# Kernel optimization log

Hardware: AMD Instinct MI355X
Metric: run time of the kernel (lower is better)

Reference implementation:

```python
import jax, jax.numpy as jnp
import numpy as np

N = 16384      # nodes
E = 524288     # edges (avg degree 32)
F_IN = 128     # input features
H1 = 256       # first_gcn_dimensions
H2 = 256       # second_gcn_dimensions
D1 = 64        # first_dense_neurons
D2 = 2         # second_dense_neurons (fixed by EYE=ones(2))


def setup_inputs() -> dict:
    key = jax.random.key(0)
    ks = jax.random.split(key, 8)
    w = lambda k, shp: (jax.random.normal(k, shp, jnp.float32) * 0.05)
    return dict(
        features=jax.random.normal(ks[0], (N, F_IN), jnp.float32),
        edges=jax.random.randint(ks[1], (2, E), 0, N),
        W1=w(ks[2], (F_IN, H1)), b1=jnp.zeros((H1,), jnp.float32),
        W2=w(ks[3], (H1, H2)), b2=jnp.zeros((H2,), jnp.float32),
        fc1_w=w(ks[4], (D1, H2)), fc1_b=jnp.zeros((D1,), jnp.float32),
        fc2_w=w(ks[5], (D2, D1)), fc2_b=jnp.zeros((D2,), jnp.float32),
    )


def gcn_conv(x, W, b, src, dst, n):
    """PyG GCNConv: xW, add self-loops, symmetric D^-1/2 (A+I) D^-1/2 aggregation."""
    x = x @ W
    loops = jnp.arange(n)
    s = jnp.concatenate([src, loops])
    d = jnp.concatenate([dst, loops])
    deg = jax.ops.segment_sum(jnp.ones(s.shape, x.dtype), d, num_segments=n)
    dinv = jnp.where(deg > 0, jax.lax.rsqrt(deg), 0.0)
    msg = x[s] * (dinv[s] * dinv[d])[:, None]          # gather + scale
    return jax.ops.segment_sum(msg, d, num_segments=n) + b  # scatter-add


def reference(features, edges, W1, b1, W2, b2, fc1_w, fc1_b, fc2_w, fc2_b):
    n = features.shape[0]
    src, dst = edges[0], edges[1]
    h1 = jax.nn.relu(gcn_conv(features, W1, b1, src, dst, n))
    h2 = gcn_conv(h1, W2, b2, src, dst, n)                 # [N, H2]
    a1 = jnp.tanh(h2 @ fc1_w.T + fc1_b)                    # [N, D1]
    assignment = jax.nn.softmax(a1 @ fc2_w.T + fc2_b, axis=1)  # [N, 2]
    group_features = assignment.T @ h2                     # [2, H2]
    # to_dense_adj: dense NxN adjacency, duplicate edges accumulate
    adj = jnp.zeros((n, n), h2.dtype).at[src, dst].add(1.0)
    new_adj = assignment.T @ (adj @ assignment)            # [2, 2]
    positive = jnp.clip(group_features[0][None, :], -100.0, 100.0)
    negative = jnp.clip(group_features[1][None, :], -100.0, 100.0)
    # F.normalize(p=1, dim=1) with eps=1e-12
    denom = jnp.maximum(jnp.sum(jnp.abs(new_adj), axis=1, keepdims=True), 1e-12)
    norm_diag = jnp.diag(new_adj / denom)
    pos_penalty = jnp.mean((norm_diag - 1.0) ** 2)         # MSE vs ones(2)
    graph_embedding = jnp.mean(group_features, axis=0, keepdims=True)  # [1, H2]
    return (graph_embedding, positive, negative, pos_penalty)
```

## Files before the change

kernel.cpp:

```cpp
#include <hip/hip_runtime.h>
#include <hip/hip_bf16.h>
#include <hip/hip_fp8.h>
#include <math.h>

#define N_NODES 16384
#define N_EDGES 524288
#define F_IN 128
#define H1 256
#define H2 256
#define D1 64
#define NA_GRID 512
#define DEG_CAP 96
#define SENT 16384

typedef __attribute__((ext_vector_type(8))) short short8;
typedef __attribute__((ext_vector_type(4))) float floatx4;
typedef unsigned short ushort_t;
typedef unsigned int uint_t;
typedef unsigned char uchar_t;

__device__ inline float bf2f(ushort_t u) {
    union { uint_t i; float f; } v;
    v.i = ((uint_t)u) << 16;
    return v.f;
}
__device__ inline ushort_t f2bs(float x) {
    __hip_bfloat16 h = __float2bfloat16(x);
    return *reinterpret_cast<ushort_t*>(&h);
}
__device__ inline uint_t pack2(float lo, float hi) {
    return (uint_t)f2bs(lo) | ((uint_t)f2bs(hi) << 16);
}
__device__ inline float f8tof(uint_t b) {
    __hip_fp8_e4m3 h; h.__x = (__hip_fp8_storage_t)(b & 0xff);
    return (float)h;
}
__device__ inline uint_t ftof8(float v) {
    __hip_fp8_e4m3 h(v);
    return (uint_t)h.__x;
}

__global__ __launch_bounds__(256) void prep_fill(
    const int* __restrict__ src, const int* __restrict__ dst,
    const float* __restrict__ W1, const float* __restrict__ W2,
    const float* __restrict__ fc1_w,
    int* __restrict__ cur, ushort_t* __restrict__ col,
    ushort_t* __restrict__ W1t, ushort_t* __restrict__ W2t,
    ushort_t* __restrict__ fc1bf) {
    int b = blockIdx.x, t = threadIdx.x;
    if (b < 2048) {
        int e = b * 256 + t;
        int d = dst[e];
        int pos = atomicAdd(&cur[d], 1);
        if (pos < DEG_CAP) col[d * DEG_CAP + pos] = (ushort_t)src[e];
    } else if (b < 2176) {
        int idx = (b - 2048) * 256 + t;
        int n = idx >> 7, k = idx & 127;
        W1t[idx] = f2bs(W1[k * 256 + n]);
    } else if (b < 2432) {
        int idx = (b - 2176) * 256 + t;
        int n = idx >> 8, k = idx & 255;
        W2t[idx] = f2bs(W2[k * 256 + n]);
    } else {
        int idx = (b - 2432) * 256 + t;
        fc1bf[idx] = f2bs(fc1_w[idx]);
    }
}

__global__ __launch_bounds__(256) void scale_feat(
    const float* __restrict__ features, const int* __restrict__ cnt,
    uchar_t* __restrict__ zs8, uchar_t* __restrict__ bufY8,
    ushort_t* __restrict__ col) {
    int b = blockIdx.x, t = threadIdx.x;
    if (b == 2048) {
        uint4 z4 = {0u, 0u, 0u, 0u};
        if (t < 8)
            *(uint4*)&zs8[(size_t)SENT * 128 + t * 16] = z4;
        else if (t >= 64 && t < 80)
            *(uint4*)&bufY8[(size_t)SENT * 256 + (t - 64) * 16] = z4;
        return;
    }
    int gid = b * 256 + t;
    int node = gid >> 5;
    int hl = gid & 31;
    int deg = cnt[node];
    float d = rsqrtf((float)(deg + 1));
    float4 v = *(const float4*)&features[gid * 4];
    uint_t p = ftof8(v.x * d) | (ftof8(v.y * d) << 8) |
               (ftof8(v.z * d) << 16) | (ftof8(v.w * d) << 24);
    *(uint_t*)&zs8[gid * 4] = p;
    if (deg < DEG_CAP) {
        int pad = (16 - (deg & 15)) & 15;
        if (hl < pad) col[node * DEG_CAP + deg + hl] = (ushort_t)SENT;
    }
}

__global__ __launch_bounds__(512, 4) void fused_layer1(
    const uchar_t* __restrict__ zs8, const int* __restrict__ cnt,
    const ushort_t* __restrict__ col, const float* __restrict__ b1,
    const ushort_t* __restrict__ W1t, const ushort_t* __restrict__ W2t,
    uchar_t* __restrict__ bufY8) {
    __shared__ __align__(16) ushort_t Az[16 * 136];
    __shared__ __align__(16) ushort_t Ah[16 * 264];
    __shared__ __align__(8) uint_t scol[768];
    const int tid = threadIdx.x;
    const int lane = tid & 63;
    const int wave = tid >> 6;
    const int m = lane & 15;
    const int quad = lane >> 4;
    const int row0 = blockIdx.x * 16;
    const uint_t* colu = (const uint_t*)col;

    if (tid < 384)
        *(uint2*)&scol[tid * 2] = *(const uint2*)&colu[row0 * 48 + tid * 2];
    __syncthreads();

    {
        const int nl0 = wave * 2, nl1 = wave * 2 + 1;
        const int node0 = row0 + nl0, node1 = row0 + nl1;
        const int foff = lane * 2;
        const int deg0 = cnt[node0], deg1 = cnt[node1];
        const int nb0 = (min(deg0, DEG_CAP) + 15) >> 4;
        const int nb1 = (min(deg1, DEG_CAP) + 15) >> 4;
        const int nbm = max(nb0, nb1);
        ushort_t s0 = *(const ushort_t*)&zs8[(size_t)node0 * 128 + foff];
        ushort_t s1 = *(const ushort_t*)&zs8[(size_t)node1 * 128 + foff];
        float a00 = f8tof(s0), a01 = f8tof(s0 >> 8);
        float a10 = f8tof(s1), a11 = f8tof(s1 >> 8);
        for (int tb = 0; tb < nbm; ++tb) {
            const bool p0 = tb < nb0, p1 = tb < nb1;
            uint_t w0[8], w1[8];
            if (p0) {
                #pragma unroll
                for (int k = 0; k < 8; ++k) w0[k] = scol[nl0 * 48 + tb * 8 + k];
            }
            if (p1) {
                #pragma unroll
                for (int k = 0; k < 8; ++k) w1[k] = scol[nl1 * 48 + tb * 8 + k];
            }
            ushort_t g0[16], g1[16];
            if (p0) {
                #pragma unroll
                for (int k = 0; k < 8; ++k) {
                    int j0 = w0[k] & 0xffff, j1 = w0[k] >> 16;
                    g0[2 * k]     = *(const ushort_t*)&zs8[(size_t)j0 * 128 + foff];
                    g0[2 * k + 1] = *(const ushort_t*)&zs8[(size_t)j1 * 128 + foff];
                }
            }
            if (p1) {
                #pragma unroll
                for (int k = 0; k < 8; ++k) {
                    int j0 = w1[k] & 0xffff, j1 = w1[k] >> 16;
                    g1[2 * k]     = *(const ushort_t*)&zs8[(size_t)j0 * 128 + foff];
                    g1[2 * k + 1] = *(const ushort_t*)&zs8[(size_t)j1 * 128 + foff];
                }
            }
            if (p0) {
                #pragma unroll
                for (int q = 0; q < 16; ++q) {
                    a00 += f8tof(g0[q]); a01 += f8tof(g0[q] >> 8);
                }
            }
            if (p1) {
                #pragma unroll
                for (int q = 0; q < 16; ++q) {
                    a10 += f8tof(g1[q]); a11 += f8tof(g1[q] >> 8);
                }
            }
        }
        float dn0 = rsqrtf((float)(deg0 + 1));
        float dn1 = rsqrtf((float)(deg1 + 1));
        *(uint_t*)&Az[nl0 * 136 + foff] = pack2(a00 * dn0, a01 * dn0);
        *(uint_t*)&Az[nl1 * 136 + foff] = pack2(a10 * dn1, a11 * dn1);
    }
    __syncthreads();

    const int wcol0 = wave * 32;
    floatx4 acc[2];
    const floatx4 zero4 = {0.f, 0.f, 0.f, 0.f};
    acc[0] = zero4; acc[1] = zero4;
    #pragma unroll
    for (int k0 = 0; k0 < 128; k0 += 32) {
        short8 a = *(const short8*)&Az[m * 136 + k0 + quad * 8];
        #pragma unroll
        for (int j = 0; j < 2; ++j) {
            short8 bb = *(const short8*)
                &W1t[(size_t)(wcol0 + j * 16 + m) * 128 + k0 + quad * 8];
            acc[j] = __builtin_amdgcn_mfma_f32_16x16x32_bf16(a, bb, acc[j], 0, 0, 0);
        }
    }
    #pragma unroll
    for (int j = 0; j < 2; ++j) {
        int cg = wcol0 + j * 16 + m;
        float bv = b1[cg];
        #pragma unroll
        for (int r = 0; r < 4; ++r) {
            float v = fmaxf(acc[j][r] + bv, 0.0f);
            Ah[(quad * 4 + r) * 264 + cg] = f2bs(v);
        }
    }
    __syncthreads();

    acc[0] = zero4; acc[1] = zero4;
    #pragma unroll
    for (int k0 = 0; k0 < 256; k0 += 32) {
        short8 a = *(const short8*)&Ah[m * 264 + k0 + quad * 8];
        #pragma unroll
        for (int j = 0; j < 2; ++j) {
            short8 bb = *(const short8*)
                &W2t[(size_t)(wcol0 + j * 16 + m) * 256 + k0 + quad * 8];
            acc[j] = __builtin_amdgcn_mfma_f32_16x16x32_bf16(a, bb, acc[j], 0, 0, 0);
        }
    }
    float rs4[4];
    #pragma unroll
    for (int r = 0; r < 4; ++r)
        rs4[r] = rsqrtf((float)(cnt[row0 + quad * 4 + r] + 1));
    #pragma unroll
    for (int j = 0; j < 2; ++j) {
        int cg = wcol0 + j * 16 + m;
        #pragma unroll
        for (int r = 0; r < 4; ++r)
            bufY8[(size_t)(row0 + quad * 4 + r) * 256 + cg] =
                (uchar_t)ftof8(acc[j][r] * rs4[r]);
    }
}

__global__ __launch_bounds__(512, 4) void fused_assign(
    const uchar_t* __restrict__ bufY8, const int* __restrict__ cnt,
    const ushort_t* __restrict__ col, const float* __restrict__ b2,
    const ushort_t* __restrict__ fc1bf, const float* __restrict__ fc1_b,
    const float* __restrict__ fc2_w, const float* __restrict__ fc2_b,
    float* __restrict__ assignp, float* __restrict__ gfr) {
    __shared__ __align__(16) ushort_t Ah[16 * 264];
    __shared__ __align__(8) uint_t scol[768];
    __shared__ float sha[16][65];
    __shared__ float sas0[16], sas1[16];
    const int tid = threadIdx.x;
    const int lane = tid & 63;
    const int wave = tid >> 6;
    const int m = lane & 15;
    const int quad = lane >> 4;
    const int row0 = blockIdx.x * 16;
    const uint_t* colu = (const uint_t*)col;

    if (tid < 384)
        *(uint2*)&scol[tid * 2] = *(const uint2*)&colu[row0 * 48 + tid * 2];
    __syncthreads();

    {
        const int nl0 = wave * 2, nl1 = wave * 2 + 1;
        const int node0 = row0 + nl0, node1 = row0 + nl1;
        const int foff = lane * 4;
        const int deg0 = cnt[node0], deg1 = cnt[node1];
        const int nb0 = (min(deg0, DEG_CAP) + 15) >> 4;
        const int nb1 = (min(deg1, DEG_CAP) + 15) >> 4;
        const int nbm = max(nb0, nb1);
        uint_t sv0 = *(const uint_t*)&bufY8[(size_t)node0 * 256 + foff];
        uint_t sv1 = *(const uint_t*)&bufY8[(size_t)node1 * 256 + foff];
        float a00 = f8tof(sv0),       a01 = f8tof(sv0 >> 8);
        float a02 = f8tof(sv0 >> 16), a03 = f8tof(sv0 >> 24);
        float a10 = f8tof(sv1),       a11 = f8tof(sv1 >> 8);
        float a12 = f8tof(sv1 >> 16), a13 = f8tof(sv1 >> 24);
        for (int tb = 0; tb < nbm; ++tb) {
            const bool p0 = tb < nb0, p1 = tb < nb1;
            uint_t w0[8], w1[8];
            if (p0) {
                #pragma unroll
                for (int k = 0; k < 8; ++k) w0[k] = scol[nl0 * 48 + tb * 8 + k];
            }
            if (p1) {
                #pragma unroll
                for (int k = 0; k < 8; ++k) w1[k] = scol[nl1 * 48 + tb * 8 + k];
            }
            uint_t g0[16], g1[16];
            if (p0) {
                #pragma unroll
                for (int k = 0; k < 8; ++k) {
                    int j0 = w0[k] & 0xffff, j1 = w0[k] >> 16;
                    g0[2 * k]     = *(const uint_t*)&bufY8[(size_t)j0 * 256 + foff];
                    g0[2 * k + 1] = *(const uint_t*)&bufY8[(size_t)j1 * 256 + foff];
                }
            }
            if (p1) {
                #pragma unroll
                for (int k = 0; k < 8; ++k) {
                    int j0 = w1[k] & 0xffff, j1 = w1[k] >> 16;
                    g1[2 * k]     = *(const uint_t*)&bufY8[(size_t)j0 * 256 + foff];
                    g1[2 * k + 1] = *(const uint_t*)&bufY8[(size_t)j1 * 256 + foff];
                }
            }
            if (p0) {
                #pragma unroll
                for (int q = 0; q < 16; ++q) {
                    a00 += f8tof(g0[q]);       a01 += f8tof(g0[q] >> 8);
                    a02 += f8tof(g0[q] >> 16); a03 += f8tof(g0[q] >> 24);
                }
            }
            if (p1) {
                #pragma unroll
                for (int q = 0; q < 16; ++q) {
                    a10 += f8tof(g1[q]);       a11 += f8tof(g1[q] >> 8);
                    a12 += f8tof(g1[q] >> 16); a13 += f8tof(g1[q] >> 24);
                }
            }
        }
        float di0 = rsqrtf((float)(deg0 + 1));
        float di1 = rsqrtf((float)(deg1 + 1));
        float4 bv = *(const float4*)&b2[foff];
        uint2 pk;
        pk.x = pack2(a00 * di0 + bv.x, a01 * di0 + bv.y);
        pk.y = pack2(a02 * di0 + bv.z, a03 * di0 + bv.w);
        *(uint2*)&Ah[nl0 * 264 + foff] = pk;
        pk.x = pack2(a10 * di1 + bv.x, a11 * di1 + bv.y);
        pk.y = pack2(a12 * di1 + bv.z, a13 * di1 + bv.w);
        *(uint2*)&Ah[nl1 * 264 + foff] = pk;
    }
    __syncthreads();

    if (wave < 4) {
        floatx4 acc = {0.f, 0.f, 0.f, 0.f};
        #pragma unroll
        for (int k0 = 0; k0 < 256; k0 += 32) {
            short8 a = *(const short8*)&Ah[m * 264 + k0 + quad * 8];
            short8 bb = *(const short8*)
                &fc1bf[(size_t)(wave * 16 + m) * 256 + k0 + quad * 8];
            acc = __builtin_amdgcn_mfma_f32_16x16x32_bf16(a, bb, acc, 0, 0, 0);
        }
        int cg = wave * 16 + m;
        float bv = fc1_b[cg];
        #pragma unroll
        for (int r = 0; r < 4; ++r)
            sha[quad * 4 + r][cg] = tanhf(acc[r] + bv);
    }
    __syncthreads();

    if (tid < 16) {
        float p0 = fc2_b[0], p1 = fc2_b[1];
        #pragma unroll 8
        for (int t = 0; t < 64; ++t) {
            float a = sha[tid][t];
            p0 += a * fc2_w[t];
            p1 += a * fc2_w[64 + t];
        }
        float mx = fmaxf(p0, p1);
        float e0 = expf(p0 - mx), e1 = expf(p1 - mx);
        float inv = 1.0f / (e0 + e1);
        assignp[row0 + tid] = e0 * inv;
        sas0[tid] = e0 * inv; sas1[tid] = e1 * inv;
    }
    __syncthreads();

    {
        const int f = tid & 255;
        const int which = tid >> 8;
        const float* sv = which ? sas1 : sas0;
        float acc = 0.f;
        #pragma unroll
        for (int i = 0; i < 16; ++i)
            acc += sv[i] * bf2f(Ah[i * 264 + f]);
        float* gfc = gfr + (blockIdx.x & 3) * 512;
        atomicAdd(&gfc[which * 256 + f], acc);
    }
}

__global__ __launch_bounds__(256) void newadj_fin(
    const int* __restrict__ src, const int* __restrict__ dst,
    const float* __restrict__ assignp, float* __restrict__ napart,
    int* __restrict__ cntt, const float* __restrict__ gfr,
    float* __restrict__ out) {
    __shared__ float red[4][3];
    __shared__ int sticket;
    const int tid = threadIdx.x;
    const int b = blockIdx.x;
    const int lane = tid & 63;
    const int wave = tid >> 6;

    float ss = 0.f, sd = 0.f, ssd = 0.f;
    {
        int g = (b * 256 + tid) * 4;
        int4 sv = *(const int4*)&src[g];
        int4 dv = *(const int4*)&dst[g];
        float s0 = assignp[sv.x], s1 = assignp[sv.y];
        float s2 = assignp[sv.z], s3 = assignp[sv.w];
        float d0 = assignp[dv.x], d1 = assignp[dv.y];
        float d2 = assignp[dv.z], d3 = assignp[dv.w];
        ss = s0 + s1 + s2 + s3;
        sd = d0 + d1 + d2 + d3;
        ssd = s0 * d0 + s1 * d1 + s2 * d2 + s3 * d3;
    }
    #pragma unroll
    for (int off = 32; off; off >>= 1) {
        ss += __shfl_down(ss, off);
        sd += __shfl_down(sd, off);
        ssd += __shfl_down(ssd, off);
    }
    if (lane == 0) {
        red[wave][0] = ssd; red[wave][1] = ss; red[wave][2] = sd;
    }
    __syncthreads();
    if (tid < 3) {
        float v = red[0][tid] + red[1][tid] + red[2][tid] + red[3][tid];
        __hip_atomic_store(&napart[b * 4 + tid], v, __ATOMIC_RELEASE,
                           __HIP_MEMORY_SCOPE_AGENT);
    }
    __syncthreads();
    if (tid == 0)
        sticket = __hip_atomic_fetch_add(cntt, 1, __ATOMIC_ACQ_REL,
                                         __HIP_MEMORY_SCOPE_AGENT);
    __syncthreads();
    if (sticket != NA_GRID - 1) return;

    float acc = 0.f;
    if (wave < 3) {
        for (int i = lane; i < NA_GRID; i += 64)
            acc += __hip_atomic_load(&napart[i * 4 + wave], __ATOMIC_RELAXED,
                                     __HIP_MEMORY_SCOPE_AGENT);
    }
    #pragma unroll
    for (int off = 32; off; off >>= 1) acc += __shfl_down(acc, off);
    __shared__ float na[3];
    if (lane == 0 && wave < 3) na[wave] = acc;
    __syncthreads();
    float g0 = gfr[tid] + gfr[512 + tid] + gfr[1024 + tid] + gfr[1536 + tid];
    float g1 = gfr[256 + tid] + gfr[768 + tid] + gfr[1280 + tid] + gfr[1792 + tid];
    out[tid] = 0.5f * (g0 + g1);
    out[256 + tid] = fminf(fmaxf(g0, -100.f), 100.f);
    out[512 + tid] = fminf(fmaxf(g1, -100.f), 100.f);
    if (tid == 0) {
        float Ssd = na[0], Ss = na[1], Sd = na[2];
        float n00 = Ssd;
        float n01 = Ss - Ssd;
        float n10 = Sd - Ssd;
        float n11 = (float)N_EDGES - Ss - Sd + Ssd;
        float den0 = fmaxf(fabsf(n00) + fabsf(n01), 1e-12f);
        float den1 = fmaxf(fabsf(n10) + fabsf(n11), 1e-12f);
        float x0 = n00 / den0 - 1.0f;
        float x1 = n11 / den1 - 1.0f;
        out[768] = 0.5f * (x0 * x0 + x1 * x1);
    }
}


extern "C" void kernel_launch(void* const* d_in, const int* in_sizes, int n_in,
                              void* d_out, int out_size, void* d_ws, size_t ws_size,
                              hipStream_t stream) {
    const float* features = (const float*)d_in[0];
    const int* edges = (const int*)d_in[1];
    const int* src = edges;
    const int* dst = edges + N_EDGES;
    const float* W1 = (const float*)d_in[2];
    const float* b1 = (const float*)d_in[3];
    const float* W2 = (const float*)d_in[4];
    const float* b2 = (const float*)d_in[5];
    const float* fc1_w = (const float*)d_in[6];
    const float* fc1_b = (const float*)d_in[7];
    const float* fc2_w = (const float*)d_in[8];
    const float* fc2_b = (const float*)d_in[9];
    float* out = (float*)d_out;

    char* ws = (char*)d_ws;
    auto carve = [&](size_t bytes) {
        void* q = (void*)ws;
        ws += (bytes + 255) & ~(size_t)255;
        return q;
    };
    int* cur = (int*)carve(N_NODES * 4);
    float* gfr = (float*)carve(4 * 512 * 4);
    int* cnt_na = (int*)carve(256);
    ushort_t* col = (ushort_t*)carve((size_t)N_NODES * DEG_CAP * 2);
    float* assignp = (float*)carve(N_NODES * 4);
    float* napart = (float*)carve(NA_GRID * 4 * 4);
    ushort_t* fc1bf = (ushort_t*)carve(64 * 256 * 2);
    uchar_t* zs8 = (uchar_t*)carve((size_t)(N_NODES + 1) * F_IN);
    ushort_t* W1t = (ushort_t*)carve(256 * 128 * 2);
    ushort_t* W2t = (ushort_t*)carve(256 * 256 * 2);
    uchar_t* bufY8 = (uchar_t*)carve((size_t)(N_NODES + 1) * 256);

    hipMemsetAsync(cur, 0, N_NODES * 4 + 4 * 512 * 4 + 256, stream);

    prep_fill<<<2496, 256, 0, stream>>>(src, dst, W1, W2, fc1_w,
                                        cur, col, W1t, W2t, fc1bf);
    scale_feat<<<2049, 256, 0, stream>>>(features, cur, zs8, bufY8, col);
    fused_layer1<<<N_NODES / 16, 512, 0, stream>>>(
        zs8, cur, col, b1, W1t, W2t, bufY8);
    fused_assign<<<N_NODES / 16, 512, 0, stream>>>(
        bufY8, cur, col, b2, fc1bf, fc1_b, fc2_w, fc2_b, assignp, gfr);
    newadj_fin<<<NA_GRID, 256, 0, stream>>>(src, dst, assignp, napart,
                                            cnt_na, gfr, out);
}
```

Before: 187.9 us.

## Fuse all stages into one cooperative persistent kernel with grid syncs

Replaces the memset plus five separate kernel launches with a single cooperative kernel of 256 blocks. The stages are CSR fill, weight conversion, feature scaling, layer1+layer2 GEMM, assignment, and the new-adjacency reduction and finalize, separated by grid.sync(). This removes launch gaps and the memset. In exchange, each persistent block loops over tiles, which reduces parallelism per stage, and six grid-wide barriers are added. The old multi-kernel path is kept as a fallback if the cooperative launch fails.

```diff
diff --git a/kernel.cpp b/kernel.cpp
--- a/kernel.cpp
+++ b/kernel.cpp
@@ -1,7 +1,10 @@
 #include <hip/hip_runtime.h>
+#include <hip/hip_cooperative_groups.h>
 #include <hip/hip_bf16.h>
 #include <hip/hip_fp8.h>
 #include <math.h>
+
+namespace cg = cooperative_groups;
 
 #define N_NODES 16384
 #define N_EDGES 524288
@@ -12,6 +15,9 @@
 #define NA_GRID 512
 #define DEG_CAP 96
 #define SENT 16384
+#define NBLK 256
+#define NTHR 512
+#define NTH (NBLK * NTHR)
 
 typedef __attribute__((ext_vector_type(8))) short short8;
 typedef __attribute__((ext_vector_type(4))) float floatx4;
@@ -39,6 +45,393 @@
     __hip_fp8_e4m3 h(v);
     return (uint_t)h.__x;
 }
+
+__global__ __launch_bounds__(512, 4) void mega(
+    const int* __restrict__ src, const int* __restrict__ dst,
+    const float* __restrict__ features,
+    const float* __restrict__ W1, const float* __restrict__ b1,
+    const float* __restrict__ W2, const float* __restrict__ b2,
+    const float* __restrict__ fc1_w, const float* __restrict__ fc1_b,
+    const float* __restrict__ fc2_w, const float* __restrict__ fc2_b,
+    int* __restrict__ cur, ushort_t* __restrict__ col,
+    float* __restrict__ assignp, float* __restrict__ napart,
+    ushort_t* __restrict__ fc1bf, uchar_t* __restrict__ zs8,
+    ushort_t* __restrict__ W1t, ushort_t* __restrict__ W2t,
+    uchar_t* __restrict__ bufY8, float* __restrict__ gfr,
+    float* __restrict__ out) {
+    cg::grid_group grid = cg::this_grid();
+    __shared__ __align__(16) ushort_t Az[16 * 136];
+    __shared__ __align__(16) ushort_t Ah[16 * 264];
+    __shared__ __align__(8) uint_t scol[768];
+    __shared__ float sha[16][65];
+    __shared__ float sas0[16], sas1[16];
+    __shared__ float red[8][3];
+
+    const int tid = threadIdx.x;
+    const int gid = blockIdx.x * NTHR + tid;
+    const int lane = tid & 63;
+    const int wave = tid >> 6;
+    const int m = lane & 15;
+    const int quad = lane >> 4;
+    const uint_t* colu = (const uint_t*)col;
+
+    if (gid < N_NODES) cur[gid] = 0;
+    else if (gid < N_NODES + 2048) gfr[gid - N_NODES] = 0.f;
+    grid.sync();
+
+    for (int e = gid; e < N_EDGES; e += NTH) {
+        int d = dst[e];
+        int pos = atomicAdd(&cur[d], 1);
+        if (pos < DEG_CAP) col[d * DEG_CAP + pos] = (ushort_t)src[e];
+    }
+    if (gid < 114688) {
+        int i = gid;
+        if (i < 32768) {
+            int n = i >> 7, k = i & 127;
+            W1t[i] = f2bs(W1[k * 256 + n]);
+        } else if (i < 98304) {
+            int j = i - 32768;
+            int n = j >> 8, k = j & 255;
+            W2t[j] = f2bs(W2[k * 256 + n]);
+        } else {
+            int j = i - 98304;
+            fc1bf[j] = f2bs(fc1_w[j]);
+        }
+    }
+    grid.sync();
+
+    if (gid < 8) {
+        uint4 z4 = {0u, 0u, 0u, 0u};
+        *(uint4*)&zs8[(size_t)SENT * 128 + gid * 16] = z4;
+    } else if (gid >= 64 && gid < 80) {
+        uint4 z4 = {0u, 0u, 0u, 0u};
+        *(uint4*)&bufY8[(size_t)SENT * 256 + (gid - 64) * 16] = z4;
+    }
+    for (int i = gid; i < 524288; i += NTH) {
+        int node = i >> 5;
+        int hl = i & 31;
+        int deg = cur[node];
+        float d = rsqrtf((float)(deg + 1));
+        float4 v = *(const float4*)&features[i * 4];
+        uint_t p = ftof8(v.x * d) | (ftof8(v.y * d) << 8) |
+                   (ftof8(v.z * d) << 16) | (ftof8(v.w * d) << 24);
+        *(uint_t*)&zs8[i * 4] = p;
+        if (deg < DEG_CAP) {
+            int pad = (16 - (deg & 15)) & 15;
+            if (hl < pad) col[node * DEG_CAP + deg + hl] = (ushort_t)SENT;
+        }
+    }
+    grid.sync();
+
+    for (int tl = blockIdx.x; tl < N_NODES / 16; tl += NBLK) {
+        const int row0 = tl * 16;
+        if (tid < 384)
+            *(uint2*)&scol[tid * 2] = *(const uint2*)&colu[row0 * 48 + tid * 2];
+        __syncthreads();
+        {
+            const int nl0 = wave * 2, nl1 = wave * 2 + 1;
+            const int node0 = row0 + nl0, node1 = row0 + nl1;
+            const int foff = lane * 2;
+            const int deg0 = cur[node0], deg1 = cur[node1];
+            const int nb0 = (min(deg0, DEG_CAP) + 15) >> 4;
+            const int nb1 = (min(deg1, DEG_CAP) + 15) >> 4;
+            const int nbm = max(nb0, nb1);
+            ushort_t s0 = *(const ushort_t*)&zs8[(size_t)node0 * 128 + foff];
+            ushort_t s1 = *(const ushort_t*)&zs8[(size_t)node1 * 128 + foff];
+            float a00 = f8tof(s0), a01 = f8tof(s0 >> 8);
+            float a10 = f8tof(s1), a11 = f8tof(s1 >> 8);
+            for (int tb = 0; tb < nbm; ++tb) {
+                const bool p0 = tb < nb0, p1 = tb < nb1;
+                uint_t w0[8], w1[8];
+                if (p0) {
+                    #pragma unroll
+                    for (int k = 0; k < 8; ++k) w0[k] = scol[nl0 * 48 + tb * 8 + k];
+                }
+                if (p1) {
+                    #pragma unroll
+                    for (int k = 0; k < 8; ++k) w1[k] = scol[nl1 * 48 + tb * 8 + k];
+                }
+                ushort_t g0[16], g1[16];
+                if (p0) {
+                    #pragma unroll
+                    for (int k = 0; k < 8; ++k) {
+                        int j0 = w0[k] & 0xffff, j1 = w0[k] >> 16;
+                        g0[2 * k]     = *(const ushort_t*)&zs8[(size_t)j0 * 128 + foff];
+                        g0[2 * k + 1] = *(const ushort_t*)&zs8[(size_t)j1 * 128 + foff];
+                    }
+                }
+                if (p1) {
+                    #pragma unroll
+                    for (int k = 0; k < 8; ++k) {
+                        int j0 = w1[k] & 0xffff, j1 = w1[k] >> 16;
+                        g1[2 * k]     = *(const ushort_t*)&zs8[(size_t)j0 * 128 + foff];
+                        g1[2 * k + 1] = *(const ushort_t*)&zs8[(size_t)j1 * 128 + foff];
+                    }
+                }
+                if (p0) {
+                    #pragma unroll
+                    for (int q = 0; q < 16; ++q) {
+                        a00 += f8tof(g0[q]); a01 += f8tof(g0[q] >> 8);
+                    }
+                }
+                if (p1) {
+                    #pragma unroll
+                    for (int q = 0; q < 16; ++q) {
+                        a10 += f8tof(g1[q]); a11 += f8tof(g1[q] >> 8);
+                    }
+                }
+            }
+            float dn0 = rsqrtf((float)(deg0 + 1));
+            float dn1 = rsqrtf((float)(deg1 + 1));
+            *(uint_t*)&Az[nl0 * 136 + foff] = pack2(a00 * dn0, a01 * dn0);
+            *(uint_t*)&Az[nl1 * 136 + foff] = pack2(a10 * dn1, a11 * dn1);
+        }
+        __syncthreads();
+        const int wcol0 = wave * 32;
+        floatx4 acc[2];
+        const floatx4 zero4 = {0.f, 0.f, 0.f, 0.f};
+        acc[0] = zero4; acc[1] = zero4;
+        #pragma unroll
+        for (int k0 = 0; k0 < 128; k0 += 32) {
+            short8 a = *(const short8*)&Az[m * 136 + k0 + quad * 8];
+            #pragma unroll
+            for (int j = 0; j < 2; ++j) {
+                short8 bb = *(const short8*)
+                    &W1t[(size_t)(wcol0 + j * 16 + m) * 128 + k0 + quad * 8];
+                acc[j] = __builtin_amdgcn_mfma_f32_16x16x32_bf16(a, bb, acc[j], 0, 0, 0);
+            }
+        }
+        #pragma unroll
+        for (int j = 0; j < 2; ++j) {
+            int cg_ = wcol0 + j * 16 + m;
+            float bv = b1[cg_];
+            #pragma unroll
+            for (int r = 0; r < 4; ++r) {
+                float v = fmaxf(acc[j][r] + bv, 0.0f);
+                Ah[(quad * 4 + r) * 264 + cg_] = f2bs(v);
+            }
+        }
+        __syncthreads();
+        acc[0] = zero4; acc[1] = zero4;
+        #pragma unroll
+        for (int k0 = 0; k0 < 256; k0 += 32) {
+            short8 a = *(const short8*)&Ah[m * 264 + k0 + quad * 8];
+            #pragma unroll
+            for (int j = 0; j < 2; ++j) {
+                short8 bb = *(const short8*)
+                    &W2t[(size_t)(wcol0 + j * 16 + m) * 256 + k0 + quad * 8];
+                acc[j] = __builtin_amdgcn_mfma_f32_16x16x32_bf16(a, bb, acc[j], 0, 0, 0);
+            }
+        }
+        float rs4[4];
+        #pragma unroll
+        for (int r = 0; r < 4; ++r)
+            rs4[r] = rsqrtf((float)(cur[row0 + quad * 4 + r] + 1));
+        #pragma unroll
+        for (int j = 0; j < 2; ++j) {
+            int cg_ = wcol0 + j * 16 + m;
+            #pragma unroll
+            for (int r = 0; r < 4; ++r)
+                bufY8[(size_t)(row0 + quad * 4 + r) * 256 + cg_] =
+                    (uchar_t)ftof8(acc[j][r] * rs4[r]);
+        }
+        __syncthreads();
+    }
+    grid.sync();
+
+    for (int tl = blockIdx.x; tl < N_NODES / 16; tl += NBLK) {
+        const int row0 = tl * 16;
+        if (tid < 384)
+            *(uint2*)&scol[tid * 2] = *(const uint2*)&colu[row0 * 48 + tid * 2];
+        __syncthreads();
+        {
+            const int nl0 = wave * 2, nl1 = wave * 2 + 1;
+            const int node0 = row0 + nl0, node1 = row0 + nl1;
+            const int foff = lane * 4;
+            const int deg0 = cur[node0], deg1 = cur[node1];
+            const int nb0 = (min(deg0, DEG_CAP) + 15) >> 4;
+            const int nb1 = (min(deg1, DEG_CAP) + 15) >> 4;
+            const int nbm = max(nb0, nb1);
+            uint_t sv0 = *(const uint_t*)&bufY8[(size_t)node0 * 256 + foff];
+            uint_t sv1 = *(const uint_t*)&bufY8[(size_t)node1 * 256 + foff];
+            float a00 = f8tof(sv0),       a01 = f8tof(sv0 >> 8);
+            float a02 = f8tof(sv0 >> 16), a03 = f8tof(sv0 >> 24);
+            float a10 = f8tof(sv1),       a11 = f8tof(sv1 >> 8);
+            float a12 = f8tof(sv1 >> 16), a13 = f8tof(sv1 >> 24);
+            for (int tb = 0; tb < nbm; ++tb) {
+                const bool p0 = tb < nb0, p1 = tb < nb1;
+                uint_t w0[8], w1[8];
+                if (p0) {
+                    #pragma unroll
+                    for (int k = 0; k < 8; ++k) w0[k] = scol[nl0 * 48 + tb * 8 + k];
+                }
+                if (p1) {
+                    #pragma unroll
+                    for (int k = 0; k < 8; ++k) w1[k] = scol[nl1 * 48 + tb * 8 + k];
+                }
+                uint_t g0[16], g1[16];
+                if (p0) {
+                    #pragma unroll
+                    for (int k = 0; k < 8; ++k) {
+                        int j0 = w0[k] & 0xffff, j1 = w0[k] >> 16;
+                        g0[2 * k]     = *(const uint_t*)&bufY8[(size_t)j0 * 256 + foff];
+                        g0[2 * k + 1] = *(const uint_t*)&bufY8[(size_t)j1 * 256 + foff];
+                    }
+                }
+                if (p1) {
+                    #pragma unroll
+                    for (int k = 0; k < 8; ++k) {
+                        int j0 = w1[k] & 0xffff, j1 = w1[k] >> 16;
+                        g1[2 * k]     = *(const uint_t*)&bufY8[(size_t)j0 * 256 + foff];
+                        g1[2 * k + 1] = *(const uint_t*)&bufY8[(size_t)j1 * 256 + foff];
+                    }
+                }
+                if (p0) {
+                    #pragma unroll
+                    for (int q = 0; q < 16; ++q) {
+                        a00 += f8tof(g0[q]);       a01 += f8tof(g0[q] >> 8);
+                        a02 += f8tof(g0[q] >> 16); a03 += f8tof(g0[q] >> 24);
+                    }
+                }
+                if (p1) {
+                    #pragma unroll
+                    for (int q = 0; q < 16; ++q) {
+                        a10 += f8tof(g1[q]);       a11 += f8tof(g1[q] >> 8);
+                        a12 += f8tof(g1[q] >> 16); a13 += f8tof(g1[q] >> 24);
+                    }
+                }
+            }
+            float di0 = rsqrtf((float)(deg0 + 1));
+            float di1 = rsqrtf((float)(deg1 + 1));
+            float4 bv = *(const float4*)&b2[foff];
+            uint2 pk;
+            pk.x = pack2(a00 * di0 + bv.x, a01 * di0 + bv.y);
+            pk.y = pack2(a02 * di0 + bv.z, a03 * di0 + bv.w);
+            *(uint2*)&Ah[nl0 * 264 + foff] = pk;
+            pk.x = pack2(a10 * di1 + bv.x, a11 * di1 + bv.y);
+            pk.y = pack2(a12 * di1 + bv.z, a13 * di1 + bv.w);
+            *(uint2*)&Ah[nl1 * 264 + foff] = pk;
+        }
+        __syncthreads();
+        if (wave < 4) {
+            floatx4 acc = {0.f, 0.f, 0.f, 0.f};
+            #pragma unroll
+            for (int k0 = 0; k0 < 256; k0 += 32) {
+                short8 a = *(const short8*)&Ah[m * 264 + k0 + quad * 8];
+                short8 bb = *(const short8*)
+                    &fc1bf[(size_t)(wave * 16 + m) * 256 + k0 + quad * 8];
+                acc = __builtin_amdgcn_mfma_f32_16x16x32_bf16(a, bb, acc, 0, 0, 0);
+            }
+            int cg_ = wave * 16 + m;
+            float bv = fc1_b[cg_];
+            #pragma unroll
+            for (int r = 0; r < 4; ++r)
+                sha[quad * 4 + r][cg_] = tanhf(acc[r] + bv);
+        }
+        __syncthreads();
+        if (tid < 16) {
+            float p0 = fc2_b[0], p1 = fc2_b[1];
+            #pragma unroll 8
+            for (int t = 0; t < 64; ++t) {
+                float a = sha[tid][t];
+                p0 += a * fc2_w[t];
+                p1 += a * fc2_w[64 + t];
+            }
+            float mx = fmaxf(p0, p1);
+            float e0 = expf(p0 - mx), e1 = expf(p1 - mx);
+            float inv = 1.0f / (e0 + e1);
+            assignp[row0 + tid] = e0 * inv;
+            sas0[tid] = e0 * inv; sas1[tid] = e1 * inv;
+        }
+        __syncthreads();
+        {
+            const int f = tid & 255;
+            const int which = tid >> 8;
+            const float* sv = which ? sas1 : sas0;
+            float acc = 0.f;
+            #pragma unroll
+            for (int i = 0; i < 16; ++i)
+                acc += sv[i] * bf2f(Ah[i * 264 + f]);
+            float* gfc = gfr + ((tl >> 2) & 3) * 512;
+            atomicAdd(&gfc[which * 256 + f], acc);
+        }
+        __syncthreads();
+    }
+    grid.sync();
+
+    {
+        int g4 = gid * 4;
+        int4 sv = *(const int4*)&src[g4];
+        int4 dv = *(const int4*)&dst[g4];
+        float s0 = assignp[sv.x], s1 = assignp[sv.y];
+        float s2 = assignp[sv.z], s3 = assignp[sv.w];
+        float d0 = assignp[dv.x], d1 = assignp[dv.y];
+        float d2 = assignp[dv.z], d3 = assignp[dv.w];
+        float ss = s0 + s1 + s2 + s3;
+        float sd = d0 + d1 + d2 + d3;
+        float ssd = s0 * d0 + s1 * d1 + s2 * d2 + s3 * d3;
+        #pragma unroll
+        for (int off = 32; off; off >>= 1) {
+            ss += __shfl_down(ss, off);
+            sd += __shfl_down(sd, off);
+            ssd += __shfl_down(ssd, off);
+        }
+        if (lane == 0) {
+            red[wave][0] = ssd; red[wave][1] = ss; red[wave][2] = sd;
+        }
+        __syncthreads();
+        if (tid < 3) {
+            float v = 0.f;
+            #pragma unroll
+            for (int w = 0; w < 8; ++w) v += red[w][tid];
+            napart[blockIdx.x * 4 + tid] = v;
+        }
+    }
+    grid.sync();
+
+    if (blockIdx.x == 0) {
+        float p0 = 0.f, p1 = 0.f, p2 = 0.f;
+        if (tid < NBLK) {
+            p0 = napart[tid * 4];
+            p1 = napart[tid * 4 + 1];
+            p2 = napart[tid * 4 + 2];
+        }
+        #pragma unroll
+        for (int off = 32; off; off >>= 1) {
+            p0 += __shfl_down(p0, off);
+            p1 += __shfl_down(p1, off);
+            p2 += __shfl_down(p2, off);
+        }
+        if (lane == 0) {
+            red[wave][0] = p0; red[wave][1] = p1; red[wave][2] = p2;
+        }
+        __syncthreads();
+        if (tid < 256) {
+            float g0 = gfr[tid] + gfr[512 + tid] + gfr[1024 + tid] + gfr[1536 + tid];
+            float g1 = gfr[256 + tid] + gfr[768 + tid] + gfr[1280 + tid] + gfr[1792 + tid];
+            out[tid] = 0.5f * (g0 + g1);
+            out[256 + tid] = fminf(fmaxf(g0, -100.f), 100.f);
+            out[512 + tid] = fminf(fmaxf(g1, -100.f), 100.f);
+        }
+        if (tid == 0) {
+            float Ssd = 0.f, Ss = 0.f, Sd = 0.f;
+            #pragma unroll
+            for (int w = 0; w < 8; ++w) {
+                Ssd += red[w][0]; Ss += red[w][1]; Sd += red[w][2];
+            }
+            float n00 = Ssd;
+            float n01 = Ss - Ssd;
+            float n10 = Sd - Ssd;
+            float n11 = (float)N_EDGES - Ss - Sd + Ssd;
+            float den0 = fmaxf(fabsf(n00) + fabsf(n01), 1e-12f);
+            float den1 = fmaxf(fabsf(n10) + fabsf(n11), 1e-12f);
+            float x0 = n00 / den0 - 1.0f;
+            float x1 = n11 / den1 - 1.0f;
+            out[768] = 0.5f * (x0 * x0 + x1 * x1);
+        }
+    }
+}
+
 
 __global__ __launch_bounds__(256) void prep_fill(
     const int* __restrict__ src, const int* __restrict__ dst,
@@ -114,7 +507,6 @@
     if (tid < 384)
         *(uint2*)&scol[tid * 2] = *(const uint2*)&colu[row0 * 48 + tid * 2];
     __syncthreads();
-
     {
         const int nl0 = wave * 2, nl1 = wave * 2 + 1;
         const int node0 = row0 + nl0, node1 = row0 + nl1;
@@ -174,7 +566,6 @@
         *(uint_t*)&Az[nl1 * 136 + foff] = pack2(a10 * dn1, a11 * dn1);
     }
     __syncthreads();
-
     const int wcol0 = wave * 32;
     floatx4 acc[2];
     const floatx4 zero4 = {0.f, 0.f, 0.f, 0.f};
@@ -191,16 +582,15 @@
     }
     #pragma unroll
     for (int j = 0; j < 2; ++j) {
-        int cg = wcol0 + j * 16 + m;
-        float bv = b1[cg];
+        int cg_ = wcol0 + j * 16 + m;
+        float bv = b1[cg_];
         #pragma unroll
         for (int r = 0; r < 4; ++r) {
             float v = fmaxf(acc[j][r] + bv, 0.0f);
-            Ah[(quad * 4 + r) * 264 + cg] = f2bs(v);
-        }
-    }
-    __syncthreads();
-
+            Ah[(quad * 4 + r) * 264 + cg_] = f2bs(v);
+        }
+    }
+    __syncthreads();
     acc[0] = zero4; acc[1] = zero4;
     #pragma unroll
     for (int k0 = 0; k0 < 256; k0 += 32) {
@@ -218,10 +608,10 @@
         rs4[r] = rsqrtf((float)(cnt[row0 + quad * 4 + r] + 1));
     #pragma unroll
     for (int j = 0; j < 2; ++j) {
-        int cg = wcol0 + j * 16 + m;
+        int cg_ = wcol0 + j * 16 + m;
         #pragma unroll
         for (int r = 0; r < 4; ++r)
-            bufY8[(size_t)(row0 + quad * 4 + r) * 256 + cg] =
+            bufY8[(size_t)(row0 + quad * 4 + r) * 256 + cg_] =
                 (uchar_t)ftof8(acc[j][r] * rs4[r]);
     }
 }
@@ -247,7 +637,6 @@
     if (tid < 384)
         *(uint2*)&scol[tid * 2] = *(const uint2*)&colu[row0 * 48 + tid * 2];
     __syncthreads();
-
     {
         const int nl0 = wave * 2, nl1 = wave * 2 + 1;
         const int node0 = row0 + nl0, node1 = row0 + nl1;
@@ -317,7 +706,6 @@
         *(uint2*)&Ah[nl1 * 264 + foff] = pk;
     }
     __syncthreads();
-
     if (wave < 4) {
         floatx4 acc = {0.f, 0.f, 0.f, 0.f};
         #pragma unroll
@@ -327,14 +715,13 @@
                 &fc1bf[(size_t)(wave * 16 + m) * 256 + k0 + quad * 8];
             acc = __builtin_amdgcn_mfma_f32_16x16x32_bf16(a, bb, acc, 0, 0, 0);
         }
-        int cg = wave * 16 + m;
-        float bv = fc1_b[cg];
+        int cg_ = wave * 16 + m;
+        float bv = fc1_b[cg_];
         #pragma unroll
         for (int r = 0; r < 4; ++r)
-            sha[quad * 4 + r][cg] = tanhf(acc[r] + bv);
-    }
-    __syncthreads();
-
+            sha[quad * 4 + r][cg_] = tanhf(acc[r] + bv);
+    }
+    __syncthreads();
     if (tid < 16) {
         float p0 = fc2_b[0], p1 = fc2_b[1];
         #pragma unroll 8
@@ -350,7 +737,6 @@
         sas0[tid] = e0 * inv; sas1[tid] = e1 * inv;
     }
     __syncthreads();
-
     {
         const int f = tid & 255;
         const int which = tid >> 8;
@@ -477,15 +863,26 @@
     ushort_t* W2t = (ushort_t*)carve(256 * 256 * 2);
     uchar_t* bufY8 = (uchar_t*)carve((size_t)(N_NODES + 1) * 256);
 
-    hipMemsetAsync(cur, 0, N_NODES * 4 + 4 * 512 * 4 + 256, stream);
-
-    prep_fill<<<2496, 256, 0, stream>>>(src, dst, W1, W2, fc1_w,
-                                        cur, col, W1t, W2t, fc1bf);
-    scale_feat<<<2049, 256, 0, stream>>>(features, cur, zs8, bufY8, col);
-    fused_layer1<<<N_NODES / 16, 512, 0, stream>>>(
-        zs8, cur, col, b1, W1t, W2t, bufY8);
-    fused_assign<<<N_NODES / 16, 512, 0, stream>>>(
-        bufY8, cur, col, b2, fc1bf, fc1_b, fc2_w, fc2_b, assignp, gfr);
-    newadj_fin<<<NA_GRID, 256, 0, stream>>>(src, dst, assignp, napart,
-                                            cnt_na, gfr, out);
-}
+    void* args[] = {
+        (void*)&src, (void*)&dst, (void*)&features,
+        (void*)&W1, (void*)&b1, (void*)&W2, (void*)&b2,
+        (void*)&fc1_w, (void*)&fc1_b, (void*)&fc2_w, (void*)&fc2_b,
+        (void*)&cur, (void*)&col, (void*)&assignp, (void*)&napart,
+        (void*)&fc1bf, (void*)&zs8, (void*)&W1t, (void*)&W2t,
+        (void*)&bufY8, (void*)&gfr, (void*)&out,
+    };
+    hipError_t err = hipLaunchCooperativeKernel((void*)mega, dim3(NBLK),
+                                                dim3(NTHR), args, 0, stream);
+    if (err != hipSuccess) {
+        hipMemsetAsync(cur, 0, N_NODES * 4 + 4 * 512 * 4 + 256, stream);
+        prep_fill<<<2496, 256, 0, stream>>>(src, dst, W1, W2, fc1_w,
+                                            cur, col, W1t, W2t, fc1bf);
+        scale_feat<<<2049, 256, 0, stream>>>(features, cur, zs8, bufY8, col);
+        fused_layer1<<<N_NODES / 16, 512, 0, stream>>>(
+            zs8, cur, col, b1, W1t, W2t, bufY8);
+        fused_assign<<<N_NODES / 16, 512, 0, stream>>>(
+            bufY8, cur, col, b2, fc1bf, fc1_b, fc2_w, fc2_b, assignp, gfr);
+        newadj_fin<<<NA_GRID, 256, 0, stream>>>(src, dst, assignp, napart,
+                                                cnt_na, gfr, out);
+    }
+}
```

Result: slower. 392.5 us (+108.9%).
